# Kernel optimization log

Measured on AMD Instinct MI355X. Metric: run time of the kernel, lower is better.

The kernel has to match this reference:

```python
import jax, jax.numpy as jnp
import numpy as np

NUM_USER = 100000
NUM_ITEM = 50000
EMBED_DIM = 64
NUM_LAYER = 3
NUM_INTERACTIONS = 1600000  # symmetrized -> nnz = 3.2M
BATCH = 4096


def setup_inputs() -> dict:
    key = jax.random.key(0)
    k1, k2, k3, k4, k5, k6 = jax.random.split(key, 6)
    N = NUM_USER + NUM_ITEM
    user_emb = jax.random.normal(k1, (NUM_USER, EMBED_DIM), dtype=jnp.float32) / EMBED_DIM
    item_emb = jax.random.normal(k2, (NUM_ITEM, EMBED_DIM), dtype=jnp.float32) / EMBED_DIM
    # random bipartite interactions, symmetrized adjacency
    u = jax.random.randint(k3, (NUM_INTERACTIONS,), 0, NUM_USER, dtype=jnp.int32)
    i = jax.random.randint(k4, (NUM_INTERACTIONS,), 0, NUM_ITEM, dtype=jnp.int32) + NUM_USER
    adj_rows = jnp.concatenate([u, i])  # [nnz]
    adj_cols = jnp.concatenate([i, u])  # [nnz]
    # symmetric normalization D^-1/2 A D^-1/2
    deg = jax.ops.segment_sum(jnp.ones_like(adj_rows, dtype=jnp.float32), adj_rows, num_segments=N)
    deg = jnp.maximum(deg, 1.0)
    inv_sqrt = 1.0 / jnp.sqrt(deg)
    adj_vals = inv_sqrt[adj_rows] * inv_sqrt[adj_cols]
    user_ids = jax.random.randint(k5, (BATCH,), 0, NUM_USER, dtype=jnp.int32)
    item_ids = jax.random.randint(k6, (BATCH,), 0, NUM_ITEM, dtype=jnp.int32)
    return {"user_emb": user_emb, "item_emb": item_emb, "adj_vals": adj_vals,
            "adj_rows": adj_rows, "adj_cols": adj_cols,
            "user_ids": user_ids, "item_ids": item_ids}


def reference(user_emb, item_emb, adj_vals, adj_rows, adj_cols, user_ids, item_ids):
    num_user = user_emb.shape[0]
    N = num_user + item_emb.shape[0]
    x = jnp.concatenate([user_emb, item_emb], axis=0)  # [N, D]
    acc = x  # running sum == stack+mean over layers, fused
    for _ in range(NUM_LAYER):
        # SpMM: out[r] += vals * x[c]
        x = jax.ops.segment_sum(adj_vals[:, None] * x[adj_cols], adj_rows, num_segments=N)
        acc = acc + x
    emb = acc / (NUM_LAYER + 1)
    batch_user = emb[user_ids]                  # [B, D]
    batch_item = emb[num_user + item_ids]       # [B, D]
    scores = jnp.sum(batch_user * batch_item, axis=-1)  # DotProdScorer
    return scores
```

## Files before the change

### kernel.cpp

```cpp
#include <hip/hip_runtime.h>


#define DIM 64
#define PW 1024
#define TSHIFT 10
#define TMASK ((1 << TSHIFT) - 1)
#define STAGE_CAP 3328
#define TSTRIDE 40960

typedef unsigned short u16;
typedef unsigned char u8;
typedef unsigned int u32;

__device__ __forceinline__ u32 f2bf(float f) {
  u32 u = __float_as_uint(f);
  return (u + 0x7FFFu + ((u >> 16) & 1u)) >> 16;
}
__device__ __forceinline__ float bflo(u32 u) {
  return __uint_as_float(u << 16);
}
__device__ __forceinline__ float bfhi(u32 u) {
  return __uint_as_float(u & 0xFFFF0000u);
}


__global__ __launch_bounds__(256) void partition_direct(
    const int* __restrict__ rows, const int* __restrict__ cols, int nnz,
    int ewg, int T, int* __restrict__ tcur, u32* __restrict__ bucket) {
  __shared__ u32 raw[STAGE_CAP];
  __shared__ u8 rawt[STAGE_CAP];
  __shared__ u32 sorted[STAGE_CAP];
  __shared__ u8 sortedt[STAGE_CAP];
  __shared__ int cnt[256], lstart[256], cur[256], sc[256], gbase[256];
  int w = blockIdx.x, tid = threadIdx.x;
  cnt[tid] = 0;
  cur[tid] = 0;
  __syncthreads();
  int base = w * ewg;
  int end = min(base + ewg, nnz);
  int total = end - base;
  for (int e = base + tid, li = tid; e < end; e += 256, li += 256) {
    int r = rows[e];
    int c = cols[e];
    int t = r >> TSHIFT;
    raw[li] = ((u32)(r & TMASK) << 18) | (u32)c;
    rawt[li] = (u8)t;
    atomicAdd(&cnt[t], 1);
  }
  __syncthreads();
  sc[tid] = cnt[tid];
  __syncthreads();
  for (int off = 1; off < 256; off <<= 1) {
    int v = (tid >= off) ? sc[tid - off] : 0;
    __syncthreads();
    sc[tid] += v;
    __syncthreads();
  }
  lstart[tid] = sc[tid] - cnt[tid];
  if (tid < T)
    gbase[tid] = tid * TSTRIDE + atomicAdd(&tcur[tid], cnt[tid]);
  __syncthreads();
  for (int li = tid; li < total; li += 256) {
    int t = rawt[li];
    int slot = atomicAdd(&cur[t], 1);
    int d = lstart[t] + slot;
    sorted[d] = raw[li];
    sortedt[d] = (u8)t;
  }
  __syncthreads();
  for (int i = tid; i < total; i += 256) {
    int t = sortedt[i];
    bucket[(size_t)gbase[t] + (i - lstart[t])] = sorted[i];
  }
}


__global__ __launch_bounds__(1024) void build_csr_y0(
    const u32* __restrict__ bucket, const int* __restrict__ tcur, int T,
    int U, int N, const float4* __restrict__ ue, const float4* __restrict__ ie,
    int* __restrict__ row_ptr, u32* __restrict__ csr,
    uint4* __restrict__ y0b) {
  __shared__ int hist[1024], sc[1024], cur[1024];
  __shared__ int tl[256];
  int t = blockIdx.x;
  int tid = threadIdx.x;
  if (tid < 256) tl[tid] = (tid < T) ? tcur[tid] : 0;
  __syncthreads();
  for (int off = 1; off < 256; off <<= 1) {
    int v = 0;
    if (tid < 256 && tid >= off) v = tl[tid - off];
    __syncthreads();
    if (tid < 256) tl[tid] += v;
    __syncthreads();
  }
  int tlen = tcur[t];
  int tbase = tl[t] - tlen;
  int bstart = t * TSTRIDE;
  hist[tid] = 0;
  __syncthreads();
  for (int e = bstart + tid; e < bstart + tlen; e += 1024)
    atomicAdd(&hist[bucket[e] >> 18], 1);
  __syncthreads();
  sc[tid] = hist[tid];
  __syncthreads();
  for (int off = 1; off < 1024; off <<= 1) {
    int v = (tid >= off) ? sc[tid - off] : 0;
    __syncthreads();
    sc[tid] += v;
    __syncthreads();
  }
  int r = (t << TSHIFT) + tid;
  if (r < N) row_ptr[r + 1] = tbase + sc[tid];
  if (t == 0 && tid == 0) row_ptr[0] = 0;
  cur[tid] = tbase + sc[tid] - hist[tid];
  __syncthreads();
  for (int pass = 0; pass < 8; ++pass) {
    int lr = pass * 128 + (tid >> 3);
    int q = tid & 7;
    int row = (t << TSHIFT) + lr;
    if (row < N) {
      float invs = rsqrtf((float)max(hist[lr], 1));
      const float4* src = (row < U) ? (ue + (size_t)row * 16 + q * 2)
                                    : (ie + (size_t)(row - U) * 16 + q * 2);
      float4 a = src[0], b = src[1];
      uint4 o;
      o.x = f2bf(a.x * invs) | (f2bf(a.y * invs) << 16);
      o.y = f2bf(a.z * invs) | (f2bf(a.w * invs) << 16);
      o.z = f2bf(b.x * invs) | (f2bf(b.y * invs) << 16);
      o.w = f2bf(b.z * invs) | (f2bf(b.w * invs) << 16);
      y0b[(size_t)row * 8 + q] = o;
    }
  }
  for (int e = bstart + tid; e < bstart + tlen; e += 1024) {
    u32 ent = bucket[e];
    int p = atomicAdd(&cur[ent >> 18], 1);
    csr[p] = ent & 0x3FFFFu;
  }
}


#define ACC8(G)                                                              \
  s0 += bflo(G.x); s1 += bfhi(G.x);                                          \
  s2 += bflo(G.y); s3 += bfhi(G.y);                                          \
  s4 += bflo(G.z); s5 += bfhi(G.z);                                          \
  s6 += bflo(G.w); s7 += bfhi(G.w);

__global__ __launch_bounds__(256) void spmm_sum(
    const int* __restrict__ row_ptr, const u32* __restrict__ csr,
    const u16* __restrict__ yin, u16* __restrict__ yout, int n) {
  if (blockIdx.x == 0 && threadIdx.x < 8)
    ((uint4*)(yout + (size_t)n * DIM))[threadIdx.x] = make_uint4(0, 0, 0, 0);
  int row = (blockIdx.x * 256 + threadIdx.x) >> 3;
  int q8 = threadIdx.x & 7;
  if (row >= n) return;
  int start = row_ptr[row];
  int end = row_ptr[row + 1];
  float s0 = 0.f, s1 = 0.f, s2 = 0.f, s3 = 0.f;
  float s4 = 0.f, s5 = 0.f, s6 = 0.f, s7 = 0.f;
  int k = start;
  for (; k + 8 <= end; k += 8) {
    u32 c0 = csr[k],     c1 = csr[k + 1], c2 = csr[k + 2], c3 = csr[k + 3];
    u32 c4 = csr[k + 4], c5 = csr[k + 5], c6 = csr[k + 6], c7 = csr[k + 7];
    uint4 g0 = ((const uint4*)(yin + (size_t)c0 * DIM))[q8];
    uint4 g1 = ((const uint4*)(yin + (size_t)c1 * DIM))[q8];
    uint4 g2 = ((const uint4*)(yin + (size_t)c2 * DIM))[q8];
    uint4 g3 = ((const uint4*)(yin + (size_t)c3 * DIM))[q8];
    uint4 g4 = ((const uint4*)(yin + (size_t)c4 * DIM))[q8];
    uint4 g5 = ((const uint4*)(yin + (size_t)c5 * DIM))[q8];
    uint4 g6 = ((const uint4*)(yin + (size_t)c6 * DIM))[q8];
    uint4 g7 = ((const uint4*)(yin + (size_t)c7 * DIM))[q8];
    ACC8(g0) ACC8(g1) ACC8(g2) ACC8(g3) ACC8(g4) ACC8(g5) ACC8(g6) ACC8(g7)
  }
  for (; k + 4 <= end; k += 4) {
    u32 c0 = csr[k], c1 = csr[k + 1], c2 = csr[k + 2], c3 = csr[k + 3];
    uint4 g0 = ((const uint4*)(yin + (size_t)c0 * DIM))[q8];
    uint4 g1 = ((const uint4*)(yin + (size_t)c1 * DIM))[q8];
    uint4 g2 = ((const uint4*)(yin + (size_t)c2 * DIM))[q8];
    uint4 g3 = ((const uint4*)(yin + (size_t)c3 * DIM))[q8];
    ACC8(g0) ACC8(g1) ACC8(g2) ACC8(g3)
  }
  for (; k < end; ++k) {
    u32 c0 = csr[k];
    uint4 g0 = ((const uint4*)(yin + (size_t)c0 * DIM))[q8];
    ACC8(g0)
  }
  float inv = 1.0f / (float)max(end - start, 1);
  uint4 o;
  o.x = f2bf(s0 * inv) | (f2bf(s1 * inv) << 16);
  o.y = f2bf(s2 * inv) | (f2bf(s3 * inv) << 16);
  o.z = f2bf(s4 * inv) | (f2bf(s5 * inv) << 16);
  o.w = f2bf(s6 * inv) | (f2bf(s7 * inv) << 16);
  ((uint4*)(yout + (size_t)row * DIM))[q8] = o;
}


__device__ __forceinline__ void gather8(
    const int* __restrict__ row_ptr, const u32* __restrict__ csr,
    const u16* __restrict__ y, int row, int s, int q8, int n, float* o) {
  int start = row_ptr[row];
  int end = row_ptr[row + 1];
  float s0 = 0.f, s1 = 0.f, s2 = 0.f, s3 = 0.f;
  float s4 = 0.f, s5 = 0.f, s6 = 0.f, s7 = 0.f;
  for (int k = start + s; k < end; k += 16) {
    int k2 = k + 8;
    bool ok2 = k2 < end;
    u32 c0 = csr[k];
    u32 c1 = ok2 ? csr[k2] : (u32)n;
    uint4 g0 = ((const uint4*)(y + (size_t)c0 * DIM))[q8];
    uint4 g1 = ((const uint4*)(y + (size_t)c1 * DIM))[q8];
    ACC8(g0) ACC8(g1)
  }
  for (int m = 8; m <= 32; m <<= 1) {
    s0 += __shfl_xor(s0, m, 64); s1 += __shfl_xor(s1, m, 64);
    s2 += __shfl_xor(s2, m, 64); s3 += __shfl_xor(s3, m, 64);
    s4 += __shfl_xor(s4, m, 64); s5 += __shfl_xor(s5, m, 64);
    s6 += __shfl_xor(s6, m, 64); s7 += __shfl_xor(s7, m, 64);
  }
  o[0] = s0; o[1] = s1; o[2] = s2; o[3] = s3;
  o[4] = s4; o[5] = s5; o[6] = s6; o[7] = s7;
}

__global__ __launch_bounds__(256) void spmm3_score(
    const int* __restrict__ row_ptr, const u32* __restrict__ csr,
    const float* __restrict__ ue, const float* __restrict__ ie,
    const u16* __restrict__ y1b, const u16* __restrict__ y2b,
    const int* __restrict__ user_ids, const int* __restrict__ item_ids,
    int U, int N, int batch, float* __restrict__ out) {
  int w = (blockIdx.x * 256 + threadIdx.x) >> 6;
  int lane = threadIdx.x & 63;
  if (w >= batch) return;
  int s = lane >> 3;
  int q8 = lane & 7;
  int u = user_ids[w];
  int iti = item_ids[w];
  int it = iti + U;
  float gu[8], gi[8];
  gather8(row_ptr, csr, y2b, u, s, q8, N, gu);
  gather8(row_ptr, csr, y2b, it, s, q8, N, gi);
  int du = row_ptr[u + 1] - row_ptr[u];
  int di = row_ptr[it + 1] - row_ptr[it];
  float su = sqrtf((float)max(du, 1)), ru = 1.0f / su;
  float si = sqrtf((float)max(di, 1)), ri = 1.0f / si;
  const float4* pu = (const float4*)(ue + (size_t)u * DIM) + q8 * 2;
  const float4* pi = (const float4*)(ie + (size_t)iti * DIM) + q8 * 2;
  float4 a0a = pu[0], a0b = pu[1];
  float4 b0a = pi[0], b0b = pi[1];
  uint4 y1u = ((const uint4*)(y1b + (size_t)u * DIM))[q8];
  uint4 y2u = ((const uint4*)(y2b + (size_t)u * DIM))[q8];
  uint4 y1i = ((const uint4*)(y1b + (size_t)it * DIM))[q8];
  uint4 y2i = ((const uint4*)(y2b + (size_t)it * DIM))[q8];
  float a[8], b[8];
  a[0] = a0a.x + su * (bflo(y1u.x) + bflo(y2u.x)) + ru * gu[0];
  a[1] = a0a.y + su * (bfhi(y1u.x) + bfhi(y2u.x)) + ru * gu[1];
  a[2] = a0a.z + su * (bflo(y1u.y) + bflo(y2u.y)) + ru * gu[2];
  a[3] = a0a.w + su * (bfhi(y1u.y) + bfhi(y2u.y)) + ru * gu[3];
  a[4] = a0b.x + su * (bflo(y1u.z) + bflo(y2u.z)) + ru * gu[4];
  a[5] = a0b.y + su * (bfhi(y1u.z) + bfhi(y2u.z)) + ru * gu[5];
  a[6] = a0b.z + su * (bflo(y1u.w) + bflo(y2u.w)) + ru * gu[6];
  a[7] = a0b.w + su * (bfhi(y1u.w) + bfhi(y2u.w)) + ru * gu[7];
  b[0] = b0a.x + si * (bflo(y1i.x) + bflo(y2i.x)) + ri * gi[0];
  b[1] = b0a.y + si * (bfhi(y1i.x) + bfhi(y2i.x)) + ri * gi[1];
  b[2] = b0a.z + si * (bflo(y1i.y) + bflo(y2i.y)) + ri * gi[2];
  b[3] = b0a.w + si * (bfhi(y1i.y) + bfhi(y2i.y)) + ri * gi[3];
  b[4] = b0b.x + si * (bflo(y1i.z) + bflo(y2i.z)) + ri * gi[4];
  b[5] = b0b.y + si * (bfhi(y1i.z) + bfhi(y2i.z)) + ri * gi[5];
  b[6] = b0b.z + si * (bflo(y1i.w) + bflo(y2i.w)) + ri * gi[6];
  b[7] = b0b.w + si * (bfhi(y1i.w) + bfhi(y2i.w)) + ri * gi[7];
  float p = 0.f;
  for (int j = 0; j < 8; ++j) p += a[j] * b[j];
  p += __shfl_xor(p, 1, 64);
  p += __shfl_xor(p, 2, 64);
  p += __shfl_xor(p, 4, 64);
  if (lane == 0) out[w] = p * (1.0f / 16.0f);
}

extern "C" void kernel_launch(void* const* d_in, const int* in_sizes, int n_in,
                              void* d_out, int out_size, void* d_ws, size_t ws_size,
                              hipStream_t stream) {
  const float* user_emb = (const float*)d_in[0];
  const float* item_emb = (const float*)d_in[1];
  const int* adj_rows = (const int*)d_in[3];
  const int* adj_cols = (const int*)d_in[4];
  const int* user_ids = (const int*)d_in[5];
  const int* item_ids = (const int*)d_in[6];
  float* scores = (float*)d_out;

  const int U = in_sizes[0] / DIM;
  const int I = in_sizes[1] / DIM;
  const int N = U + I;
  const int nnz = in_sizes[2];
  const int B = in_sizes[5];

  const int T = (N + TMASK) >> TSHIFT;
  const int ewg = (nnz + PW - 1) / PW;

  char* p = (char*)d_ws;
  auto carve = [&](size_t bytes) {
    void* r = (void*)p;
    p += (bytes + 255) & ~(size_t)255;
    return r;
  };
  u16* y0b = (u16*)carve((size_t)(N + 1) * DIM * 2);
  u16* y1b = (u16*)carve((size_t)(N + 1) * DIM * 2);
  u16* y2b = (u16*)carve((size_t)(N + 1) * DIM * 2);
  int* row_ptr = (int*)carve((size_t)(N + 1) * 4);
  int* tcur = (int*)carve((size_t)T * 4);
  u32* bucket = (u32*)carve((size_t)(T + 1) * TSTRIDE * 4);
  u32* csr = (u32*)carve((size_t)nnz * 4);

  hipMemsetAsync(tcur, 0, (size_t)T * 4, stream);

  partition_direct<<<PW, 256, 0, stream>>>(adj_rows, adj_cols, nnz, ewg, T,
                                           tcur, bucket);

  build_csr_y0<<<T, 1024, 0, stream>>>(bucket, tcur, T, U, N,
                                       (const float4*)user_emb,
                                       (const float4*)item_emb, row_ptr, csr,
                                       (uint4*)y0b);

  const int sblocks = (N * 8 + 255) / 256;
  spmm_sum<<<sblocks, 256, 0, stream>>>(row_ptr, csr, y0b, y1b, N);
  spmm_sum<<<sblocks, 256, 0, stream>>>(row_ptr, csr, y1b, y2b, N);

  spmm3_score<<<(B + 3) / 4, 256, 0, stream>>>(row_ptr, csr, user_emb,
                                               item_emb, y1b, y2b, user_ids,
                                               item_ids, U, N, B, scores);
}
```

Baseline: 295.6 us.

## Split CSR build into quarter-tile blocks and separate y0 scaling kernel

The single 1024-thread-per-tile CSR build kernel is replaced by four 256-thread blocks per tile. Each block recomputes the full tile histogram but scatters only the rows of its quarter, and uses vectorized uint4 bucket reads. The y0 bf16 scaling moves into its own fully parallel kernel that reads degrees from row_ptr. The intent is more blocks for occupancy (T is small, about 147) at the cost of reading each bucket four times and one extra launch.

```diff
diff --git a/kernel.cpp b/kernel.cpp
--- a/kernel.cpp
+++ b/kernel.cpp
@@ -75,67 +75,116 @@
 }
 
 
-__global__ __launch_bounds__(1024) void build_csr_y0(
+__global__ __launch_bounds__(256) void build_csr(
     const u32* __restrict__ bucket, const int* __restrict__ tcur, int T,
-    int U, int N, const float4* __restrict__ ue, const float4* __restrict__ ie,
-    int* __restrict__ row_ptr, u32* __restrict__ csr,
-    uint4* __restrict__ y0b) {
-  __shared__ int hist[1024], sc[1024], cur[1024];
+    int N, int* __restrict__ row_ptr, u32* __restrict__ csr) {
   __shared__ int tl[256];
-  int t = blockIdx.x;
+  __shared__ int hist[1024];
+  __shared__ int hsum[256];
+  __shared__ int cur[256];
+  int b = blockIdx.x;
+  int t = b >> 2;
+  int qt = b & 3;
   int tid = threadIdx.x;
-  if (tid < 256) tl[tid] = (tid < T) ? tcur[tid] : 0;
+  tl[tid] = (tid < T) ? tcur[tid] : 0;
   __syncthreads();
   for (int off = 1; off < 256; off <<= 1) {
-    int v = 0;
-    if (tid < 256 && tid >= off) v = tl[tid - off];
-    __syncthreads();
-    if (tid < 256) tl[tid] += v;
-    __syncthreads();
-  }
-  int tlen = tcur[t];
-  int tbase = tl[t] - tlen;
+    int v = (tid >= off) ? tl[tid - off] : 0;
+    __syncthreads();
+    tl[tid] += v;
+    __syncthreads();
+  }
+  int tbase = (t == 0) ? 0 : tl[t - 1];
+  int tlen = tl[t] - tbase;
   int bstart = t * TSTRIDE;
   hist[tid] = 0;
-  __syncthreads();
-  for (int e = bstart + tid; e < bstart + tlen; e += 1024)
-    atomicAdd(&hist[bucket[e] >> 18], 1);
-  __syncthreads();
-  sc[tid] = hist[tid];
-  __syncthreads();
-  for (int off = 1; off < 1024; off <<= 1) {
-    int v = (tid >= off) ? sc[tid - off] : 0;
-    __syncthreads();
-    sc[tid] += v;
-    __syncthreads();
-  }
-  int r = (t << TSHIFT) + tid;
-  if (r < N) row_ptr[r + 1] = tbase + sc[tid];
-  if (t == 0 && tid == 0) row_ptr[0] = 0;
-  cur[tid] = tbase + sc[tid] - hist[tid];
-  __syncthreads();
-  for (int pass = 0; pass < 8; ++pass) {
-    int lr = pass * 128 + (tid >> 3);
-    int q = tid & 7;
-    int row = (t << TSHIFT) + lr;
-    if (row < N) {
-      float invs = rsqrtf((float)max(hist[lr], 1));
-      const float4* src = (row < U) ? (ue + (size_t)row * 16 + q * 2)
-                                    : (ie + (size_t)(row - U) * 16 + q * 2);
-      float4 a = src[0], b = src[1];
-      uint4 o;
-      o.x = f2bf(a.x * invs) | (f2bf(a.y * invs) << 16);
-      o.y = f2bf(a.z * invs) | (f2bf(a.w * invs) << 16);
-      o.z = f2bf(b.x * invs) | (f2bf(b.y * invs) << 16);
-      o.w = f2bf(b.z * invs) | (f2bf(b.w * invs) << 16);
-      y0b[(size_t)row * 8 + q] = o;
-    }
-  }
-  for (int e = bstart + tid; e < bstart + tlen; e += 1024) {
-    u32 ent = bucket[e];
-    int p = atomicAdd(&cur[ent >> 18], 1);
-    csr[p] = ent & 0x3FFFFu;
-  }
+  hist[tid + 256] = 0;
+  hist[tid + 512] = 0;
+  hist[tid + 768] = 0;
+  __syncthreads();
+  const uint4* b4 = (const uint4*)(bucket + bstart);
+  int nv = tlen >> 2;
+  for (int i = tid; i < nv; i += 256) {
+    uint4 e = b4[i];
+    atomicAdd(&hist[e.x >> 18], 1);
+    atomicAdd(&hist[e.y >> 18], 1);
+    atomicAdd(&hist[e.z >> 18], 1);
+    atomicAdd(&hist[e.w >> 18], 1);
+  }
+  for (int i = bstart + (nv << 2) + tid; i < bstart + tlen; i += 256)
+    atomicAdd(&hist[bucket[i] >> 18], 1);
+  __syncthreads();
+  int h0 = hist[tid * 4], h1 = hist[tid * 4 + 1];
+  int h2 = hist[tid * 4 + 2], h3 = hist[tid * 4 + 3];
+  int lsum = h0 + h1 + h2 + h3;
+  hsum[tid] = lsum;
+  __syncthreads();
+  for (int off = 1; off < 256; off <<= 1) {
+    int v = (tid >= off) ? hsum[tid - off] : 0;
+    __syncthreads();
+    hsum[tid] += v;
+    __syncthreads();
+  }
+  int excl = hsum[tid] - lsum;
+  int o0 = excl + h0, o1 = o0 + h1, o2 = o1 + h2, o3 = o2 + h3;
+  if (qt == 0) {
+    int r = (t << TSHIFT) + tid * 4;
+    if (r + 0 < N) row_ptr[r + 1] = tbase + o0;
+    if (r + 1 < N) row_ptr[r + 2] = tbase + o1;
+    if (r + 2 < N) row_ptr[r + 3] = tbase + o2;
+    if (r + 3 < N) row_ptr[r + 4] = tbase + o3;
+    if (t == 0 && tid == 0) row_ptr[0] = 0;
+  }
+  if ((tid >> 6) == qt) {
+    int lq = (tid & 63) * 4;
+    cur[lq + 0] = tbase + o0 - h0;
+    cur[lq + 1] = tbase + o1 - h1;
+    cur[lq + 2] = tbase + o2 - h2;
+    cur[lq + 3] = tbase + o3 - h3;
+  }
+  __syncthreads();
+  for (int i = tid; i < nv; i += 256) {
+    uint4 e = b4[i];
+    int lr;
+    lr = e.x >> 18;
+    if ((lr >> 8) == qt) csr[atomicAdd(&cur[lr & 255], 1)] = e.x & 0x3FFFFu;
+    lr = e.y >> 18;
+    if ((lr >> 8) == qt) csr[atomicAdd(&cur[lr & 255], 1)] = e.y & 0x3FFFFu;
+    lr = e.z >> 18;
+    if ((lr >> 8) == qt) csr[atomicAdd(&cur[lr & 255], 1)] = e.z & 0x3FFFFu;
+    lr = e.w >> 18;
+    if ((lr >> 8) == qt) csr[atomicAdd(&cur[lr & 255], 1)] = e.w & 0x3FFFFu;
+  }
+  for (int i = bstart + (nv << 2) + tid; i < bstart + tlen; i += 256) {
+    u32 e = bucket[i];
+    int lr = e >> 18;
+    if ((lr >> 8) == qt) csr[atomicAdd(&cur[lr & 255], 1)] = e & 0x3FFFFu;
+  }
+}
+
+
+__global__ __launch_bounds__(256) void make_y0(
+    const float4* __restrict__ ue, const float4* __restrict__ ie, int U,
+    int N, const int* __restrict__ row_ptr, uint4* __restrict__ y0b) {
+  int i = blockIdx.x * 256 + threadIdx.x;
+  int n8 = (N + 1) * 8;
+  if (i >= n8) return;
+  int row = i >> 3, q = i & 7;
+  if (row == N) {
+    y0b[i] = make_uint4(0, 0, 0, 0);
+    return;
+  }
+  int deg = row_ptr[row + 1] - row_ptr[row];
+  float invs = rsqrtf((float)max(deg, 1));
+  const float4* src = (row < U) ? (ue + (size_t)row * 16 + q * 2)
+                                : (ie + (size_t)(row - U) * 16 + q * 2);
+  float4 a = src[0], b = src[1];
+  uint4 o;
+  o.x = f2bf(a.x * invs) | (f2bf(a.y * invs) << 16);
+  o.y = f2bf(a.z * invs) | (f2bf(a.w * invs) << 16);
+  o.z = f2bf(b.x * invs) | (f2bf(b.y * invs) << 16);
+  o.w = f2bf(b.z * invs) | (f2bf(b.w * invs) << 16);
+  y0b[i] = o;
 }
 
 
@@ -313,10 +362,12 @@
   partition_direct<<<PW, 256, 0, stream>>>(adj_rows, adj_cols, nnz, ewg, T,
                                            tcur, bucket);
 
-  build_csr_y0<<<T, 1024, 0, stream>>>(bucket, tcur, T, U, N,
-                                       (const float4*)user_emb,
-                                       (const float4*)item_emb, row_ptr, csr,
-                                       (uint4*)y0b);
+  build_csr<<<T * 4, 256, 0, stream>>>(bucket, tcur, T, N, row_ptr, csr);
+
+  const int n8 = (N + 1) * 8;
+  make_y0<<<(n8 + 255) / 256, 256, 0, stream>>>(
+      (const float4*)user_emb, (const float4*)item_emb, U, N, row_ptr,
+      (uint4*)y0b);
 
   const int sblocks = (N * 8 + 255) / 256;
   spmm_sum<<<sblocks, 256, 0, stream>>>(row_ptr, csr, y0b, y1b, N);
```

Result: faster. 286.1 us (-3.2%).
